# Optimization experiments

Measured on AMD Instinct MI355X. Metric: run time of the kernel, lower is better.

Reference implementation:

```python
import jax, jax.numpy as jnp
import numpy as np

G, N, F_IN, H, C = 128, 256, 128, 256, 10   # graphs, nodes/graph, in-feat, hidden, classes
NUM_NODES = G * N                            # 32768
E = NUM_NODES * 16                           # 524288 edges (avg degree 16)
K1, K2, K3 = 128, 64, 32                     # ceil(0.5*N) pooling chain per graph


def setup_inputs():
    key = jax.random.key(0)
    ks = jax.random.split(key, 16)
    def lin(k, fi, fo):
        return (jax.random.normal(k, (fi, fo), jnp.float32) / np.sqrt(fi).astype(np.float32))
    x = jax.random.normal(ks[0], (NUM_NODES, F_IN), jnp.float32)
    gid = jnp.repeat(jnp.arange(G), E // G)
    src = (gid * N + jax.random.randint(ks[1], (E,), 0, N)).astype(jnp.int32)
    dst = (gid * N + jax.random.randint(ks[2], (E,), 0, N)).astype(jnp.int32)
    edge_index = jnp.stack([src, dst])
    batch = jnp.repeat(jnp.arange(G), N).astype(jnp.int32)
    z32 = lambda *s: jnp.zeros(s, jnp.float32)
    return dict(
        x=x, edge_index=edge_index, batch=batch,
        conv1_W=lin(ks[3], F_IN, H), conv1_b=z32(H),
        conv2_W=lin(ks[4], H, H), conv2_b=z32(H),
        conv3_W=lin(ks[5], H, H), conv3_b=z32(H),
        pool1_rel_W=lin(ks[6], H, 1), pool1_rel_b=z32(1), pool1_root_W=lin(ks[7], H, 1),
        pool2_rel_W=lin(ks[8], H, 1), pool2_rel_b=z32(1), pool2_root_W=lin(ks[9], H, 1),
        fc1_W=lin(ks[10], 3 * H, H), fc1_b=z32(H),
        fc2_W=lin(ks[11], H, H // 2), fc2_b=z32(H // 2),
        fc3_W=lin(ks[12], H // 2, C), fc3_b=z32(C))


def _gcn(x, W, b, src, dst, emask, nmask):
    # PyG GCNConv: out = D^{-1/2}(A+I)D^{-1/2} (x W) + b, masked nodes/edges excluded.
    h = x @ W
    ew = emask.astype(x.dtype)
    deg = jax.ops.segment_sum(ew, dst, num_segments=NUM_NODES) + nmask  # +1 self-loop for active nodes
    dis = jnp.where(deg > 0, jax.lax.rsqrt(jnp.maximum(deg, 1e-12)), 0.0)
    norm = dis[src] * dis[dst] * ew
    out = jax.ops.segment_sum(h[src] * norm[:, None], dst, num_segments=NUM_NODES)
    out = out + h * (dis * dis * nmask)[:, None]  # self-loop message
    return out + b


def _sag_pool(x, src, dst, emask, nmask, k, w_rel, b_rel, w_root):
    # score = GraphConv(x): lin_root(x) + lin_rel(sum_j x_j); then top-k per graph, x *= tanh(score)
    ew = emask.astype(x.dtype)
    agg = jax.ops.segment_sum(x[src] * ew[:, None], dst, num_segments=NUM_NODES)
    score = (agg @ w_rel + b_rel + x @ w_root)[:, 0]
    score = jnp.where(nmask > 0, score, -jnp.inf)
    _, idx = jax.lax.top_k(score.reshape(G, N), k)           # [G, k] within-graph indices
    newmask = jnp.zeros((G, N), x.dtype).at[jnp.arange(G)[:, None], idx].set(1.0).reshape(-1)
    x = x * jnp.tanh(score)[:, None] * newmask[:, None]
    emask = emask & (newmask[src] > 0) & (newmask[dst] > 0)
    return x, emask, newmask


def _readout(x, nmask):
    xg = x.reshape(G, N, -1)
    m = nmask.reshape(G, N, 1)
    s = (xg * m).sum(axis=1)                                  # add-pool
    mean = s / m.sum(axis=1)                                  # mean-pool
    mx = jnp.max(jnp.where(m > 0, xg, -jnp.inf), axis=1)      # max-pool
    return jnp.concatenate([mean, mx, s], axis=-1)            # [G, 3H]


def reference(x, edge_index, batch, conv1_W, conv1_b, conv2_W, conv2_b, conv3_W, conv3_b,
              pool1_rel_W, pool1_rel_b, pool1_root_W, pool2_rel_W, pool2_rel_b, pool2_root_W,
              fc1_W, fc1_b, fc2_W, fc2_b, fc3_W, fc3_b):
    src, dst = edge_index[0], edge_index[1]
    nmask = jnp.ones((NUM_NODES,), x.dtype)
    emask = jnp.ones((E,), bool)
    h = jax.nn.relu(_gcn(x, conv1_W, conv1_b, src, dst, emask, nmask))
    h, emask, nmask = _sag_pool(h, src, dst, emask, nmask, K1, pool1_rel_W, pool1_rel_b, pool1_root_W)
    x1 = _readout(h, nmask)
    h = jax.nn.relu(_gcn(h, conv2_W, conv2_b, src, dst, emask, nmask))
    h, emask, nmask = _sag_pool(h, src, dst, emask, nmask, K2, pool2_rel_W, pool2_rel_b, pool2_root_W)
    x2 = _readout(h, nmask)
    h = jax.nn.relu(_gcn(h, conv3_W, conv3_b, src, dst, emask, nmask))
    # NB: original source reuses self.pool2 for the third pooling stage
    h, emask, nmask = _sag_pool(h, src, dst, emask, nmask, K3, pool2_rel_W, pool2_rel_b, pool2_root_W)
    x3 = _readout(h, nmask)
    z = x1 + x2 + x3
    z = jax.nn.relu(z @ fc1_W + fc1_b)
    z = jax.nn.relu(z @ fc2_W + fc2_b)          # dropout is identity in eval mode
    return jax.nn.log_softmax(z @ fc3_W + fc3_b, axis=-1)
```

## Files before the change

### kernel.cpp

```cpp
#include <hip/hip_runtime.h>
#include <math.h>

#define NG 128
#define NPG 256
#define NN 32768
#define HDIM 256
#define FIN 128

__global__ __launch_bounds__(256) void k_csr(const int* __restrict__ esrc,
                                             const int* __restrict__ edst, int EPG,
                                             int* __restrict__ rowptr, int* __restrict__ csr) {
    __shared__ int cnt[NPG];
    __shared__ int pref[NPG];
    __shared__ int cur[NPG];
    int g = blockIdx.x, tid = threadIdx.x;
    cnt[tid] = 0;
    __syncthreads();
    int base = g * EPG;
    for (int e = base + tid; e < base + EPG; e += 256)
        atomicAdd(&cnt[edst[e] & (NPG - 1)], 1);
    __syncthreads();
    int v = cnt[tid];
    pref[tid] = v;
    __syncthreads();
    for (int off = 1; off < NPG; off <<= 1) {
        int t = (tid >= off) ? pref[tid - off] : 0;
        __syncthreads();
        pref[tid] += t;
        __syncthreads();
    }
    int excl = pref[tid] - v;
    rowptr[g * NPG + tid] = base + excl;
    cur[tid] = base + excl;
    if (g == 0 && tid == 0) rowptr[NN] = NG * EPG;
    __syncthreads();
    for (int e = base + tid; e < base + EPG; e += 256) {
        int d = edst[e] & (NPG - 1);
        int p = atomicAdd(&cur[d], 1);
        csr[p] = esrc[e];
    }
}

__device__ __forceinline__ int swz_block(int bid, int bpg) {
    int xcd = bid & 7, r = bid >> 3;
    int graph = xcd * (NG / 8) + r / bpg;
    int sub = r - (r / bpg) * bpg;
    return graph * bpg + sub;
}

__global__ __launch_bounds__(256) void k_sortagg(const float* __restrict__ x,
                                                 const int* __restrict__ rowptr,
                                                 int* __restrict__ csr,
                                                 float* __restrict__ xa) {
    __shared__ int skey[4][64];
    __shared__ float swgt[4][64];
    int blk = swz_block(blockIdx.x, NPG / 4);
    int w = threadIdx.x >> 6, lane = threadIdx.x & 63;
    int n = blk * 4 + w;
    int e0 = rowptr[n];
    int d = rowptr[n + 1] - e0;
    float ddst = rsqrtf((float)(1 + d));
    bool big = d > 64;
    if (!big) {
        int key = (lane < d) ? csr[e0 + lane] : 0x7fffffff;
        int rank = 0;
        for (int j = 0; j < d; j++) {
            int kj = __shfl(key, j);
            rank += (kj < key || (kj == key && j < lane)) ? 1 : 0;
        }
        if (lane < d) {
            csr[e0 + rank] = key;
            skey[w][rank] = key;
            swgt[w][rank] = rsqrtf((float)(1 + rowptr[key + 1] - rowptr[key])) * ddst;
        }
    } else if (lane == 0) {
        for (int a = e0 + 1; a < e0 + d; a++) {
            int key = csr[a];
            int b = a - 1;
            while (b >= e0 && csr[b] > key) { csr[b + 1] = csr[b]; b--; }
            csr[b + 1] = key;
        }
    }
    __syncthreads();
    const float2* x2 = reinterpret_cast<const float2*>(x);
    float di = ddst;
    float2 h = x2[(size_t)n * (FIN / 2) + lane];
    float self = di * di;
    float ax = h.x * self, ay = h.y * self;
    if (!big) {
        for (int j = 0; j < d; j++) {
            int s = skey[w][j];
            float we = swgt[w][j];
            float2 hs = x2[(size_t)s * (FIN / 2) + lane];
            ax += hs.x * we; ay += hs.y * we;
        }
    } else {
        for (int e = e0; e < e0 + d; e++) {
            int s = csr[e];
            float we = rsqrtf((float)(1 + rowptr[s + 1] - rowptr[s])) * ddst;
            float2 hs = x2[(size_t)s * (FIN / 2) + lane];
            ax += hs.x * we; ay += hs.y * we;
        }
    }
    float2 o; o.x = ax; o.y = ay;
    reinterpret_cast<float2*>(xa)[(size_t)n * (FIN / 2) + lane] = o;
}

#define BM 64
#define BN 64
#define BK 16
#define BMP 68
__global__ __launch_bounds__(256) void k_sgemm(const float* __restrict__ A,
                                               const float* __restrict__ B,
                                               float* __restrict__ C, int K,
                                               const int* __restrict__ list,
                                               const float* __restrict__ brelu,
                                               const float* __restrict__ wrel,
                                               const float* __restrict__ wroot,
                                               float* __restrict__ rrel4,
                                               float* __restrict__ rroot4) {
    const int N = HDIM;
    __shared__ float As[BK][BMP];
    __shared__ float Bs[BK][BN];
    int tid = threadIdx.x;
    int tx = tid & 15, ty = tid >> 4;
    int row0 = blockIdx.y * BM, col0 = blockIdx.x * BN;
    int lm = tid >> 2;
    int arow = list ? list[row0 + lm] : (row0 + lm);
    int crow[4];
#pragma unroll
    for (int i = 0; i < 4; i++) {
        int r = row0 + ty * 4 + i;
        crow[i] = list ? list[r] : r;
    }
    int k4 = (tid & 3) * 4;
    int kkB = tid >> 4, cB = (tid & 15) * 4;
    float4 aP = *reinterpret_cast<const float4*>(&A[(size_t)arow * K + k4]);
    float4 bP = *reinterpret_cast<const float4*>(&B[(size_t)kkB * N + col0 + cB]);
    float acc[4][4] = {};
    for (int kb = 0; kb < K; kb += BK) {
        As[k4 + 0][lm] = aP.x; As[k4 + 1][lm] = aP.y;
        As[k4 + 2][lm] = aP.z; As[k4 + 3][lm] = aP.w;
        *reinterpret_cast<float4*>(&Bs[kkB][cB]) = bP;
        __syncthreads();
        if (kb + BK < K) {
            aP = *reinterpret_cast<const float4*>(&A[(size_t)arow * K + kb + BK + k4]);
            bP = *reinterpret_cast<const float4*>(&B[(size_t)(kb + BK + kkB) * N + col0 + cB]);
        }
#pragma unroll
        for (int k = 0; k < BK; k++) {
            float4 a = *reinterpret_cast<float4*>(&As[k][ty * 4]);
            float4 b = *reinterpret_cast<float4*>(&Bs[k][tx * 4]);
            float av[4] = {a.x, a.y, a.z, a.w};
            float bv[4] = {b.x, b.y, b.z, b.w};
#pragma unroll
            for (int i = 0; i < 4; i++)
#pragma unroll
                for (int j = 0; j < 4; j++) acc[i][j] += av[i] * bv[j];
        }
        __syncthreads();
    }
    float4 bb = make_float4(0.f, 0.f, 0.f, 0.f);
    if (brelu) bb = *reinterpret_cast<const float4*>(&brelu[col0 + tx * 4]);
    float4 wr = make_float4(0.f, 0.f, 0.f, 0.f), wo = wr;
    if (wrel) {
        wr = *reinterpret_cast<const float4*>(&wrel[col0 + tx * 4]);
        wo = *reinterpret_cast<const float4*>(&wroot[col0 + tx * 4]);
    }
#pragma unroll
    for (int i = 0; i < 4; i++) {
        float4 v = make_float4(acc[i][0], acc[i][1], acc[i][2], acc[i][3]);
        if (brelu) {
            v.x = fmaxf(v.x + bb.x, 0.f);
            v.y = fmaxf(v.y + bb.y, 0.f);
            v.z = fmaxf(v.z + bb.z, 0.f);
            v.w = fmaxf(v.w + bb.w, 0.f);
        }
        *reinterpret_cast<float4*>(&C[(size_t)crow[i] * N + col0 + tx * 4]) = v;
        if (wrel) {
            float s1 = v.x * wr.x + v.y * wr.y + v.z * wr.z + v.w * wr.w;
            float s2 = v.x * wo.x + v.y * wo.y + v.z * wo.z + v.w * wo.w;
            for (int off = 8; off > 0; off >>= 1) {
                s1 += __shfl_down(s1, off, 16);
                s2 += __shfl_down(s2, off, 16);
            }
            if (tx == 0) {
                rrel4[(size_t)crow[i] * 4 + blockIdx.x] = s1;
                rroot4[(size_t)crow[i] * 4 + blockIdx.x] = s2;
            }
        }
    }
}

__global__ __launch_bounds__(256) void k_gcn_agg(const float* __restrict__ hW,
                                                 const float* __restrict__ dis,
                                                 const int* __restrict__ rowptr,
                                                 const int* __restrict__ csr,
                                                 const float* __restrict__ wedge,
                                                 const float* __restrict__ bias,
                                                 const int* __restrict__ list, int bpg,
                                                 const float* __restrict__ w_rel,
                                                 const float* __restrict__ w_root,
                                                 float* __restrict__ out,
                                                 float* __restrict__ r_rel,
                                                 float* __restrict__ r_root) {
    int blk = swz_block(blockIdx.x, bpg);
    int idx = blk * 4 + (threadIdx.x >> 6);
    int lane = threadIdx.x & 63;
    int wid = list[idx];
    float di = dis[wid];
    float4 h = *reinterpret_cast<const float4*>(&hW[(size_t)wid * HDIM + lane * 4]);
    float self = di * di;
    float ax = h.x * self, ay = h.y * self, az = h.z * self, aw = h.w * self;
    int e0 = rowptr[wid], e1 = rowptr[wid + 1];
    for (int e = e0; e < e1; e++) {
        float w = wedge[e];
        if (w > 0.f) {
            int s = csr[e];
            float4 hs = *reinterpret_cast<const float4*>(&hW[(size_t)s * HDIM + lane * 4]);
            ax += hs.x * w; ay += hs.y * w; az += hs.z * w; aw += hs.w * w;
        }
    }
    float4 b = *reinterpret_cast<const float4*>(&bias[lane * 4]);
    float4 o;
    o.x = fmaxf(ax + b.x, 0.f);
    o.y = fmaxf(ay + b.y, 0.f);
    o.z = fmaxf(az + b.z, 0.f);
    o.w = fmaxf(aw + b.w, 0.f);
    *reinterpret_cast<float4*>(&out[(size_t)wid * HDIM + lane * 4]) = o;
    float4 wr = *reinterpret_cast<const float4*>(&w_rel[lane * 4]);
    float4 wo = *reinterpret_cast<const float4*>(&w_root[lane * 4]);
    float s1 = o.x * wr.x + o.y * wr.y + o.z * wr.z + o.w * wr.w;
    float s2 = o.x * wo.x + o.y * wo.y + o.z * wo.z + o.w * wo.w;
    for (int off = 32; off > 0; off >>= 1) {
        s1 += __shfl_down(s1, off);
        s2 += __shfl_down(s2, off);
    }
    if (lane == 0) { r_rel[wid] = s1; r_root[wid] = s2; }
}

template<bool STAGE1, bool EMIT, bool FIRST>
__global__ __launch_bounds__(256) void k_topkpool(const float* __restrict__ dis,
                                                  const int* __restrict__ rowptr,
                                                  const int* __restrict__ csr,
                                                  const float* __restrict__ r_rel,
                                                  const float* __restrict__ r_root,
                                                  const float* __restrict__ rrel4,
                                                  const float* __restrict__ rroot4,
                                                  const float* __restrict__ b_rel, int k,
                                                  int* __restrict__ list,
                                                  float* __restrict__ h,
                                                  float* __restrict__ z, float invk,
                                                  float* __restrict__ disN,
                                                  float* __restrict__ wedgeN) {
    __shared__ float rrel[NPG];
    __shared__ float sc[NPG];
    __shared__ int pref[NPG];
    __shared__ int sels[NPG];
    __shared__ float disn[NPG];
    __shared__ int newl[128];
    __shared__ float tvsel[128];
    __shared__ float red_s[4][64];
    __shared__ float red_m[4][64];
    int g = blockIdx.x >> 2, fc = blockIdx.x & 3;
    int tid = threadIdx.x;
    int n = g * NPG + tid;
    bool act = STAGE1 ? true : (dis[n] > 0.f);
    float rr, ro;
    if (STAGE1) {
        rr = ((rrel4[(size_t)n * 4 + 0] + rrel4[(size_t)n * 4 + 1]) +
              rrel4[(size_t)n * 4 + 2]) + rrel4[(size_t)n * 4 + 3];
        ro = ((rroot4[(size_t)n * 4 + 0] + rroot4[(size_t)n * 4 + 1]) +
              rroot4[(size_t)n * 4 + 2]) + rroot4[(size_t)n * 4 + 3];
    } else {
        rr = act ? r_rel[n] : 0.f;
        ro = act ? r_root[n] : 0.f;
    }
    rrel[tid] = act ? rr : 0.f;
    __syncthreads();
    int e0 = rowptr[n], e1 = rowptr[n + 1];
    float my;
    if (act) {
        float s = b_rel[0] + ro;
        for (int e = e0; e < e1; e++) s += rrel[csr[e] & (NPG - 1)];
        my = s;
    } else {
        my = -INFINITY;
    }
    sc[tid] = my;
    __syncthreads();
    int cnt = 0;
    for (int j = 0; j < NPG; j++) {
        float v = sc[j];
        cnt += (v > my || (v == my && j < tid)) ? 1 : 0;
    }
    int a = (cnt < k) ? 1 : 0;
    sels[tid] = a;
    pref[tid] = a;
    __syncthreads();
    for (int off = 1; off < NPG; off <<= 1) {
        int v = (tid >= off) ? pref[tid - off] : 0;
        __syncthreads();
        pref[tid] += v;
        __syncthreads();
    }
    if (a) {
        int rk = pref[tid] - 1;
        newl[rk] = tid;
        tvsel[rk] = tanhf(my);
        if (fc == 0 && list) list[g * k + rk] = n;
    }
    if (EMIT) {
        int c2 = 1;
        for (int e = e0; e < e1; e++) c2 += sels[csr[e] & (NPG - 1)];
        float dn = a ? rsqrtf((float)c2) : 0.f;
        disn[tid] = dn;
        if (fc == 0) disN[n] = dn;
        __syncthreads();
        if (a && fc == 0) {
            for (int e = e0; e < e1; e++) wedgeN[e] = disn[csr[e] & (NPG - 1)] * dn;
        }
    }
    __syncthreads();
    int xq = tid & 63, y = tid >> 6;
    int f = fc * 64 + xq;
    float s = 0.f, mx = -INFINITY;
    for (int idx = y; idx < k; idx += 4) {
        int node = g * NPG + newl[idx];
        size_t p = (size_t)node * HDIM + f;
        float v = h[p] * tvsel[idx];
        h[p] = v;
        s += v;
        mx = fmaxf(mx, v);
    }
    red_s[y][xq] = s;
    red_m[y][xq] = mx;
    __syncthreads();
    if (y == 0) {
        s = red_s[0][xq] + red_s[1][xq] + red_s[2][xq] + red_s[3][xq];
        mx = fmaxf(fmaxf(red_m[0][xq], red_m[1][xq]), fmaxf(red_m[2][xq], red_m[3][xq]));
        if (FIRST) {
            z[g * 768 + f] = s * invk;
            z[g * 768 + 256 + f] = mx;
            z[g * 768 + 512 + f] = s;
        } else {
            z[g * 768 + f] += s * invk;
            z[g * 768 + 256 + f] += mx;
            z[g * 768 + 512 + f] += s;
        }
    }
}

__global__ __launch_bounds__(256) void k_mlp(const float* __restrict__ z,
                                             const float* __restrict__ W1, const float* __restrict__ b1,
                                             const float* __restrict__ W2, const float* __restrict__ b2,
                                             const float* __restrict__ W3, const float* __restrict__ b3,
                                             float* __restrict__ out) {
    __shared__ float zb[768];
    __shared__ float t1[256];
    __shared__ float t2[128];
    __shared__ float t3[10];
    __shared__ float lse;
    int g = blockIdx.x, tid = threadIdx.x;
    zb[tid] = z[g * 768 + tid];
    zb[tid + 256] = z[g * 768 + 256 + tid];
    zb[tid + 512] = z[g * 768 + 512 + tid];
    __syncthreads();
    {
        int col = tid;
        float r0 = 0.f, r1 = 0.f, r2 = 0.f, r3 = 0.f;
        for (int i = 0;   i < 192; i++) r0 += zb[i] * W1[(size_t)i * 256 + col];
        for (int i = 192; i < 384; i++) r1 += zb[i] * W1[(size_t)i * 256 + col];
        for (int i = 384; i < 576; i++) r2 += zb[i] * W1[(size_t)i * 256 + col];
        for (int i = 576; i < 768; i++) r3 += zb[i] * W1[(size_t)i * 256 + col];
        t1[col] = fmaxf(r0 + r1 + r2 + r3 + b1[col], 0.f);
    }
    __syncthreads();
    if (tid < 128) {
        int col = tid;
        float r0 = 0.f, r1 = 0.f, r2 = 0.f, r3 = 0.f;
        for (int i = 0;   i < 64;  i++) r0 += t1[i] * W2[(size_t)i * 128 + col];
        for (int i = 64;  i < 128; i++) r1 += t1[i] * W2[(size_t)i * 128 + col];
        for (int i = 128; i < 192; i++) r2 += t1[i] * W2[(size_t)i * 128 + col];
        for (int i = 192; i < 256; i++) r3 += t1[i] * W2[(size_t)i * 128 + col];
        t2[col] = fmaxf(((r0 + r1) + r2) + r3 + b2[col], 0.f);
    }
    __syncthreads();
    if (tid < 10) {
        float v = b3[tid];
        for (int i = 0; i < 128; i++) v += t2[i] * W3[(size_t)i * 10 + tid];
        t3[tid] = v;
    }
    __syncthreads();
    if (tid == 0) {
        float m = t3[0];
        for (int c = 1; c < 10; c++) m = fmaxf(m, t3[c]);
        float se = 0.f;
        for (int c = 0; c < 10; c++) se += expf(t3[c] - m);
        lse = m + logf(se);
    }
    __syncthreads();
    if (tid < 10) out[g * 10 + tid] = t3[tid] - lse;
}

extern "C" void kernel_launch(void* const* d_in, const int* in_sizes, int n_in,
                              void* d_out, int out_size, void* d_ws, size_t ws_size,
                              hipStream_t stream) {
    const float* x        = (const float*)d_in[0];
    const int*   ei       = (const int*)d_in[1];
    const float* conv1_W  = (const float*)d_in[3];
    const float* conv1_b  = (const float*)d_in[4];
    const float* conv2_W  = (const float*)d_in[5];
    const float* conv2_b  = (const float*)d_in[6];
    const float* conv3_W  = (const float*)d_in[7];
    const float* conv3_b  = (const float*)d_in[8];
    const float* p1_relW  = (const float*)d_in[9];
    const float* p1_relb  = (const float*)d_in[10];
    const float* p1_rootW = (const float*)d_in[11];
    const float* p2_relW  = (const float*)d_in[12];
    const float* p2_relb  = (const float*)d_in[13];
    const float* p2_rootW = (const float*)d_in[14];
    const float* fc1_W    = (const float*)d_in[15];
    const float* fc1_b    = (const float*)d_in[16];
    const float* fc2_W    = (const float*)d_in[17];
    const float* fc2_b    = (const float*)d_in[18];
    const float* fc3_W    = (const float*)d_in[19];
    const float* fc3_b    = (const float*)d_in[20];
    float* out = (float*)d_out;

    const int E = in_sizes[1] / 2;
    const int EPG = E / NG;
    const int* e_src = ei;
    const int* e_dst = ei + E;

    char* base = (char*)d_ws;
    size_t off = 0;
    auto alloc = [&](size_t bytes) { size_t o = off; off = (off + bytes + 255) & ~(size_t)255; return o; };
    float* hW     = (float*)(base + alloc((size_t)NN * HDIM * 4));
    float* hcur   = (float*)(base + alloc((size_t)NN * HDIM * 4));
    float* dis    = (float*)(base + alloc(NN * 4));
    float* dis2   = (float*)(base + alloc(NN * 4));
    float* r_rel  = (float*)(base + alloc(NN * 4));
    float* r_root = (float*)(base + alloc(NN * 4));
    float* rrel4  = (float*)(base + alloc((size_t)NN * 4 * 4));
    float* rroot4 = (float*)(base + alloc((size_t)NN * 4 * 4));
    int*   rowptr = (int*)(base + alloc((NN + 1) * 4));
    int*   csr    = (int*)(base + alloc((size_t)E * 4));
    float* wedge  = (float*)(base + alloc((size_t)E * 4));
    float* z      = (float*)(base + alloc((size_t)NG * 768 * 4));
    int*   list1  = (int*)(base + alloc((size_t)NG * 128 * 4));
    int*   list2  = (int*)(base + alloc((size_t)NG * 64 * 4));

    k_csr<<<NG, 256, 0, stream>>>(e_src, e_dst, EPG, rowptr, csr);
    float* xa = hW;
    k_sortagg<<<NN / 4, 256, 0, stream>>>(x, rowptr, csr, xa);

    {
        dim3 ggrid(HDIM / BN, NN / BM);
        k_sgemm<<<ggrid, 256, 0, stream>>>(xa, conv1_W, hcur, FIN, nullptr, conv1_b,
                                           p1_relW, p1_rootW, rrel4, rroot4);
    }
    k_topkpool<true, true, true><<<NG * 4, 256, 0, stream>>>(
        nullptr, rowptr, csr, nullptr, nullptr, rrel4, rroot4, p1_relb, 128,
        list1, hcur, z, 1.0f / 128.0f, dis, wedge);

    {
        dim3 ggrid(HDIM / BN, (NG * 128) / BM);
        k_sgemm<<<ggrid, 256, 0, stream>>>(hcur, conv2_W, hW, HDIM, list1, nullptr,
                                           nullptr, nullptr, nullptr, nullptr);
    }
    k_gcn_agg<<<(NG * 128) / 4, 256, 0, stream>>>(hW, dis, rowptr, csr, wedge, conv2_b,
                                                  list1, 32, p2_relW, p2_rootW,
                                                  hcur, r_rel, r_root);
    k_topkpool<false, true, false><<<NG * 4, 256, 0, stream>>>(
        dis, rowptr, csr, r_rel, r_root, nullptr, nullptr, p2_relb, 64,
        list2, hcur, z, 1.0f / 64.0f, dis2, wedge);

    {
        dim3 ggrid(HDIM / BN, (NG * 64) / BM);
        k_sgemm<<<ggrid, 256, 0, stream>>>(hcur, conv3_W, hW, HDIM, list2, nullptr,
                                           nullptr, nullptr, nullptr, nullptr);
    }
    k_gcn_agg<<<(NG * 64) / 4, 256, 0, stream>>>(hW, dis2, rowptr, csr, wedge, conv3_b,
                                                 list2, 16, p2_relW, p2_rootW,
                                                 hcur, r_rel, r_root);
    k_topkpool<false, false, false><<<NG * 4, 256, 0, stream>>>(
        dis2, rowptr, csr, r_rel, r_root, nullptr, nullptr, p2_relb, 32,
        nullptr, hcur, z, 1.0f / 32.0f, nullptr, nullptr);

    k_mlp<<<NG, 256, 0, stream>>>(z, fc1_W, fc1_b, fc2_W, fc2_b, fc3_W, fc3_b, out);
}
```

Before: 294.1 us.

## Compact CSR to surviving edges after each pooling stage

```diff
diff --git a/kernel.cpp b/kernel.cpp
--- a/kernel.cpp
+++ b/kernel.cpp
@@ -194,9 +194,10 @@
 
 __global__ __launch_bounds__(256) void k_gcn_agg(const float* __restrict__ hW,
                                                  const float* __restrict__ dis,
-                                                 const int* __restrict__ rowptr,
-                                                 const int* __restrict__ csr,
-                                                 const float* __restrict__ wedge,
+                                                 const int* __restrict__ rs,
+                                                 const int* __restrict__ re,
+                                                 const int* __restrict__ ccsr,
+                                                 const float* __restrict__ cwedge,
                                                  const float* __restrict__ bias,
                                                  const int* __restrict__ list, int bpg,
                                                  const float* __restrict__ w_rel,
@@ -212,14 +213,12 @@
     float4 h = *reinterpret_cast<const float4*>(&hW[(size_t)wid * HDIM + lane * 4]);
     float self = di * di;
     float ax = h.x * self, ay = h.y * self, az = h.z * self, aw = h.w * self;
-    int e0 = rowptr[wid], e1 = rowptr[wid + 1];
+    int e0 = rs[wid], e1 = re[wid];
     for (int e = e0; e < e1; e++) {
-        float w = wedge[e];
-        if (w > 0.f) {
-            int s = csr[e];
-            float4 hs = *reinterpret_cast<const float4*>(&hW[(size_t)s * HDIM + lane * 4]);
-            ax += hs.x * w; ay += hs.y * w; az += hs.z * w; aw += hs.w * w;
-        }
+        float w = cwedge[e];
+        int s = ccsr[e];
+        float4 hs = *reinterpret_cast<const float4*>(&hW[(size_t)s * HDIM + lane * 4]);
+        ax += hs.x * w; ay += hs.y * w; az += hs.z * w; aw += hs.w * w;
     }
     float4 b = *reinterpret_cast<const float4*>(&bias[lane * 4]);
     float4 o;
@@ -241,8 +240,9 @@
 
 template<bool STAGE1, bool EMIT, bool FIRST>
 __global__ __launch_bounds__(256) void k_topkpool(const float* __restrict__ dis,
-                                                  const int* __restrict__ rowptr,
-                                                  const int* __restrict__ csr,
+                                                  const int* __restrict__ rs,
+                                                  const int* __restrict__ re,
+                                                  const int* __restrict__ csr_in,
                                                   const float* __restrict__ r_rel,
                                                   const float* __restrict__ r_root,
                                                   const float* __restrict__ rrel4,
@@ -252,7 +252,11 @@
                                                   float* __restrict__ h,
                                                   float* __restrict__ z, float invk,
                                                   float* __restrict__ disN,
-                                                  float* __restrict__ wedgeN) {
+                                                  int* __restrict__ csN,
+                                                  int* __restrict__ ceN,
+                                                  int* __restrict__ ccsrN,
+                                                  float* __restrict__ cwedgeN,
+                                                  int EPG) {
     __shared__ float rrel[NPG];
     __shared__ float sc[NPG];
     __shared__ int pref[NPG];
@@ -278,11 +282,11 @@
     }
     rrel[tid] = act ? rr : 0.f;
     __syncthreads();
-    int e0 = rowptr[n], e1 = rowptr[n + 1];
+    int e0 = rs[n], e1 = re[n];
     float my;
     if (act) {
         float s = b_rel[0] + ro;
-        for (int e = e0; e < e1; e++) s += rrel[csr[e] & (NPG - 1)];
+        for (int e = e0; e < e1; e++) s += rrel[csr_in[e] & (NPG - 1)];
         my = s;
     } else {
         my = -INFINITY;
@@ -311,14 +315,38 @@
         if (fc == 0 && list) list[g * k + rk] = n;
     }
     if (EMIT) {
-        int c2 = 1;
-        for (int e = e0; e < e1; e++) c2 += sels[csr[e] & (NPG - 1)];
-        float dn = a ? rsqrtf((float)c2) : 0.f;
+        int deg2 = 0;
+        if (a) {
+            for (int e = e0; e < e1; e++) deg2 += sels[csr_in[e] & (NPG - 1)];
+        }
+        float dn = a ? rsqrtf((float)(1 + deg2)) : 0.f;
         disn[tid] = dn;
-        if (fc == 0) disN[n] = dn;
-        __syncthreads();
-        if (a && fc == 0) {
-            for (int e = e0; e < e1; e++) wedgeN[e] = disn[csr[e] & (NPG - 1)] * dn;
+        __syncthreads();
+        pref[tid] = deg2;
+        __syncthreads();
+        for (int off = 1; off < NPG; off <<= 1) {
+            int v = (tid >= off) ? pref[tid - off] : 0;
+            __syncthreads();
+            pref[tid] += v;
+            __syncthreads();
+        }
+        if (fc == 0) {
+            disN[n] = dn;
+            int start = g * EPG + pref[tid] - deg2;
+            csN[n] = start;
+            ceN[n] = start + deg2;
+            if (a) {
+                int p = start;
+                for (int e = e0; e < e1; e++) {
+                    int srcg = csr_in[e];
+                    int j = srcg & (NPG - 1);
+                    if (sels[j]) {
+                        ccsrN[p] = srcg;
+                        cwedgeN[p] = disn[j] * dn;
+                        p++;
+                    }
+                }
+            }
         }
     }
     __syncthreads();
@@ -446,7 +474,14 @@
     float* rroot4 = (float*)(base + alloc((size_t)NN * 4 * 4));
     int*   rowptr = (int*)(base + alloc((NN + 1) * 4));
     int*   csr    = (int*)(base + alloc((size_t)E * 4));
-    float* wedge  = (float*)(base + alloc((size_t)E * 4));
+    int*   cs1    = (int*)(base + alloc(NN * 4));
+    int*   ce1    = (int*)(base + alloc(NN * 4));
+    int*   ccsr1  = (int*)(base + alloc((size_t)E * 4));
+    float* cwdg1  = (float*)(base + alloc((size_t)E * 4));
+    int*   cs2    = (int*)(base + alloc(NN * 4));
+    int*   ce2    = (int*)(base + alloc(NN * 4));
+    int*   ccsr2  = (int*)(base + alloc((size_t)E * 4));
+    float* cwdg2  = (float*)(base + alloc((size_t)E * 4));
     float* z      = (float*)(base + alloc((size_t)NG * 768 * 4));
     int*   list1  = (int*)(base + alloc((size_t)NG * 128 * 4));
     int*   list2  = (int*)(base + alloc((size_t)NG * 64 * 4));
@@ -461,32 +496,32 @@
                                            p1_relW, p1_rootW, rrel4, rroot4);
     }
     k_topkpool<true, true, true><<<NG * 4, 256, 0, stream>>>(
-        nullptr, rowptr, csr, nullptr, nullptr, rrel4, rroot4, p1_relb, 128,
-        list1, hcur, z, 1.0f / 128.0f, dis, wedge);
+        nullptr, rowptr, rowptr + 1, csr, nullptr, nullptr, rrel4, rroot4, p1_relb, 128,
+        list1, hcur, z, 1.0f / 128.0f, dis, cs1, ce1, ccsr1, cwdg1, EPG);
 
     {
         dim3 ggrid(HDIM / BN, (NG * 128) / BM);
         k_sgemm<<<ggrid, 256, 0, stream>>>(hcur, conv2_W, hW, HDIM, list1, nullptr,
                                            nullptr, nullptr, nullptr, nullptr);
     }
-    k_gcn_agg<<<(NG * 128) / 4, 256, 0, stream>>>(hW, dis, rowptr, csr, wedge, conv2_b,
+    k_gcn_agg<<<(NG * 128) / 4, 256, 0, stream>>>(hW, dis, cs1, ce1, ccsr1, cwdg1, conv2_b,
                                                   list1, 32, p2_relW, p2_rootW,
                                                   hcur, r_rel, r_root);
     k_topkpool<false, true, false><<<NG * 4, 256, 0, stream>>>(
-        dis, rowptr, csr, r_rel, r_root, nullptr, nullptr, p2_relb, 64,
-        list2, hcur, z, 1.0f / 64.0f, dis2, wedge);
+        dis, cs1, ce1, ccsr1, r_rel, r_root, nullptr, nullptr, p2_relb, 64,
+        list2, hcur, z, 1.0f / 64.0f, dis2, cs2, ce2, ccsr2, cwdg2, EPG);
 
     {
         dim3 ggrid(HDIM / BN, (NG * 64) / BM);
         k_sgemm<<<ggrid, 256, 0, stream>>>(hcur, conv3_W, hW, HDIM, list2, nullptr,
                                            nullptr, nullptr, nullptr, nullptr);
     }
-    k_gcn_agg<<<(NG * 64) / 4, 256, 0, stream>>>(hW, dis2, rowptr, csr, wedge, conv3_b,
+    k_gcn_agg<<<(NG * 64) / 4, 256, 0, stream>>>(hW, dis2, cs2, ce2, ccsr2, cwdg2, conv3_b,
                                                  list2, 16, p2_relW, p2_rootW,
                                                  hcur, r_rel, r_root);
     k_topkpool<false, false, false><<<NG * 4, 256, 0, stream>>>(
-        dis2, rowptr, csr, r_rel, r_root, nullptr, nullptr, p2_relb, 32,
-        nullptr, hcur, z, 1.0f / 32.0f, nullptr, nullptr);
+        dis2, cs2, ce2, ccsr2, r_rel, r_root, nullptr, nullptr, p2_relb, 32,
+        nullptr, hcur, z, 1.0f / 32.0f, nullptr, nullptr, nullptr, nullptr, nullptr, EPG);
 
     k_mlp<<<NG, 256, 0, stream>>>(z, fc1_W, fc1_b, fc2_W, fc2_b, fc3_W, fc3_b, out);
 }
```

After: 281.2 us. -4.4%, faster.
